# Kernel tuning notes

Measured on AMD Instinct MI355X. Metric: run time of the kernel, lower is better.

## Reference

```python
import jax, jax.numpy as jnp
import numpy as np

E = 400000          # total child edges in the ready batch
P = 100000          # number of parent nodes (segments)
D = 256             # 2 * model_dim


def setup_inputs() -> dict:
    key = jax.random.key(0)
    ks = jax.random.split(key, 6)
    child_hs = jax.random.normal(ks[0], (E, D), dtype=jnp.float32)
    child_cs = jax.random.normal(ks[1], (E, D), dtype=jnp.float32)
    segment_ids = jnp.sort(jax.random.randint(ks[2], (E,), 0, P))
    W_gates = jax.random.normal(ks[3], (D, 3 * D), dtype=jnp.float32) * (1.0 / np.sqrt(D))
    b_gates = jnp.zeros((3 * D,), dtype=jnp.float32)
    W_f = jax.random.normal(ks[4], (D, D), dtype=jnp.float32) * (1.0 / np.sqrt(D))
    b_f = jnp.zeros((D,), dtype=jnp.float32)
    return {
        "child_hs": child_hs,
        "child_cs": child_cs,
        "segment_ids": segment_ids,
        "num_segments": P,
        "W_gates": W_gates,
        "b_gates": b_gates,
        "W_f": W_f,
        "b_f": b_f,
    }


def reference(child_hs, child_cs, segment_ids, num_segments, W_gates, b_gates, W_f, b_f):
    # child_hs_sum per parent (segment reduce over children)
    hs_sum = jax.ops.segment_sum(child_hs, segment_ids, num_segments=num_segments)  # [P, D]
    # gates = Linear(2*model_dim -> 6*model_dim), chunk into i, o, g
    gates = hs_sum @ W_gates + b_gates                         # [P, 3D]
    i, o, g = jnp.split(gates, 3, axis=1)
    i, o, g = jax.nn.sigmoid(i), jax.nn.sigmoid(o), jnp.tanh(g)
    # per-child forget gates, fc = f * c, segment-reduced per parent
    f = jax.nn.sigmoid(child_hs @ W_f + b_f)                   # [E, D]
    fc = jax.ops.segment_sum(f * child_cs, segment_ids, num_segments=num_segments)  # [P, D]
    # child-sum LSTM update
    c = i * g + fc
    h = o * jnp.tanh(c)
    return h, c
```

## Files before the change

### kernel.cpp

```cpp
#include <hip/hip_runtime.h>
#include <hip/hip_bf16.h>

typedef __attribute__((ext_vector_type(8))) short short8;
typedef __attribute__((ext_vector_type(4))) float floatx4;

#define DD 256

__device__ __forceinline__ unsigned short f2bf(float f) {
    unsigned int u = __builtin_bit_cast(unsigned int, f);
    u += 0x7FFFu + ((u >> 16) & 1u);
    return (unsigned short)(u >> 16);
}

__device__ __forceinline__ float sigm(float x) { return 1.0f / (1.0f + __expf(-x)); }
__device__ __forceinline__ float tanh_fast(float x) { return 2.0f / (1.0f + __expf(-2.0f * x)) - 1.0f; }

__global__ void pack_weights(const float* __restrict__ W_f, const float* __restrict__ W_g,
                             unsigned short* __restrict__ WfT, unsigned short* __restrict__ WgT) {
    int idx = blockIdx.x * 256 + threadIdx.x;
    if (idx < 65536) {
        int n = idx >> 8, k = idx & 255;
        WfT[idx] = f2bf(W_f[k * 256 + n]);
    } else {
        int i2 = idx - 65536;
        int n = i2 >> 8, k = i2 & 255;
        WgT[i2] = f2bf(W_g[k * 768 + n]);
    }
}

__global__ void build_start(const int* __restrict__ seg, int E, int P, int* __restrict__ start) {
    int e = blockIdx.x * blockDim.x + threadIdx.x;
    if (e >= E) return;
    int s = seg[e];
    if (e == 0) {
        for (int p = 0; p <= s; ++p) start[p] = 0;
    } else {
        int sp = seg[e - 1];
        for (int p = sp + 1; p <= s; ++p) start[p] = e;
    }
    if (e == E - 1) {
        for (int p = s + 1; p <= P; ++p) start[p] = E;
    }
}

__global__ void hs_reduce(const float* __restrict__ child_hs, const int* __restrict__ start,
                          int P, float* __restrict__ hs_sum) {
    int wave = threadIdx.x >> 6, lane = threadIdx.x & 63;
    int p = blockIdx.x * 4 + wave;
    if (p >= P) return;
    int lo = start[p], hi = start[p + 1];
    float4 acc = make_float4(0.f, 0.f, 0.f, 0.f);
    const float4* src = (const float4*)child_hs;
    for (int e = lo; e < hi; ++e) {
        float4 v = src[(size_t)e * 64 + lane];
        acc.x += v.x; acc.y += v.y; acc.z += v.z; acc.w += v.w;
    }
    ((float4*)hs_sum)[(size_t)p * 64 + lane] = acc;
}

__global__ __launch_bounds__(256, 2) void gemm1_fc(
    const float* __restrict__ child_hs, const float* __restrict__ child_cs,
    const int* __restrict__ seg, const unsigned short* __restrict__ WfT,
    const float* __restrict__ b_f, float* __restrict__ fc, int E) {
    __shared__ __align__(16) unsigned short ldsB[8192];
    const int tid = threadIdx.x;
    const int w = tid >> 6, lane = tid & 63;
    const int nl = lane & 15, q = lane >> 4;
    const int e_base = blockIdx.x * 64 + w * 16;

    floatx4 acc[16];
#pragma unroll
    for (int t = 0; t < 16; ++t) acc[t] = (floatx4){0.f, 0.f, 0.f, 0.f};

    const float* Arow = child_hs + (size_t)(e_base + nl) * DD;

    for (int ks = 0; ks < 8; ++ks) {
#pragma unroll
        for (int r = 0; r < 4; ++r) {
            int chunk = tid + r * 256;
            int n = chunk >> 2, qb = chunk & 3;
            uint4 v = *(const uint4*)(WfT + n * 256 + ks * 32 + qb * 8);
            int dst = ((n >> 4) << 6) + (qb << 4) + (n & 15);
            ((uint4*)ldsB)[dst] = v;
        }
        float4 a0 = *(const float4*)(Arow + ks * 32 + q * 8);
        float4 a1 = *(const float4*)(Arow + ks * 32 + q * 8 + 4);
        short8 af;
        af[0] = (short)f2bf(a0.x); af[1] = (short)f2bf(a0.y);
        af[2] = (short)f2bf(a0.z); af[3] = (short)f2bf(a0.w);
        af[4] = (short)f2bf(a1.x); af[5] = (short)f2bf(a1.y);
        af[6] = (short)f2bf(a1.z); af[7] = (short)f2bf(a1.w);
        __syncthreads();
#pragma unroll
        for (int t = 0; t < 16; ++t) {
            short8 bf = ((const short8*)ldsB)[t * 64 + lane];
            acc[t] = __builtin_amdgcn_mfma_f32_16x16x32_bf16(af, bf, acc[t], 0, 0, 0);
        }
        __syncthreads();
    }

    int e0 = e_base + q * 4;
    int s0 = seg[e0], s1 = seg[e0 + 1], s2 = seg[e0 + 2], s3 = seg[e0 + 3];
#pragma unroll
    for (int t = 0; t < 16; ++t) {
        int n = t * 16 + nl;
        float bias = b_f[n];
        float v0 = sigm(acc[t][0] + bias) * child_cs[(size_t)(e0 + 0) * DD + n];
        float v1 = sigm(acc[t][1] + bias) * child_cs[(size_t)(e0 + 1) * DD + n];
        float v2 = sigm(acc[t][2] + bias) * child_cs[(size_t)(e0 + 2) * DD + n];
        float v3 = sigm(acc[t][3] + bias) * child_cs[(size_t)(e0 + 3) * DD + n];
        float a = v0; int s = s0;
        if (s1 == s) { a += v1; } else { atomicAdd(&fc[(size_t)s * DD + n], a); a = v1; s = s1; }
        if (s2 == s) { a += v2; } else { atomicAdd(&fc[(size_t)s * DD + n], a); a = v2; s = s2; }
        if (s3 == s) { a += v3; } else { atomicAdd(&fc[(size_t)s * DD + n], a); a = v3; s = s3; }
        atomicAdd(&fc[(size_t)s * DD + n], a);
    }
}

__global__ __launch_bounds__(512, 2) void gemm2_lstm(
    const float* __restrict__ hs_sum, const unsigned short* __restrict__ WgT,
    const float* __restrict__ b_g, float* __restrict__ h_out, float* __restrict__ c_out, int P) {
    __shared__ __align__(16) unsigned short ldsB[24576];
    const int tid = threadIdx.x;
    const int w = tid >> 6, lane = tid & 63;
    const int wr = w >> 2, wc = w & 3;
    const int nl = lane & 15, q = lane >> 4;
    const int p_base = blockIdx.x * 64;

    floatx4 acc[2][12];
#pragma unroll
    for (int rt = 0; rt < 2; ++rt)
#pragma unroll
        for (int t = 0; t < 12; ++t) acc[rt][t] = (floatx4){0.f, 0.f, 0.f, 0.f};

    const float* Arow0 = hs_sum + (size_t)(p_base + wr * 32 + nl) * DD;
    const float* Arow1 = Arow0 + (size_t)16 * DD;

    for (int ks = 0; ks < 8; ++ks) {
#pragma unroll
        for (int r = 0; r < 6; ++r) {
            int chunk = tid + r * 512;
            int n = chunk >> 2, qb = chunk & 3;
            uint4 v = *(const uint4*)(WgT + n * 256 + ks * 32 + qb * 8);
            int dst = ((n >> 4) << 6) + (qb << 4) + (n & 15);
            ((uint4*)ldsB)[dst] = v;
        }
        float4 a0 = *(const float4*)(Arow0 + ks * 32 + q * 8);
        float4 a1 = *(const float4*)(Arow0 + ks * 32 + q * 8 + 4);
        float4 a2 = *(const float4*)(Arow1 + ks * 32 + q * 8);
        float4 a3 = *(const float4*)(Arow1 + ks * 32 + q * 8 + 4);
        short8 af0, af1;
        af0[0] = (short)f2bf(a0.x); af0[1] = (short)f2bf(a0.y);
        af0[2] = (short)f2bf(a0.z); af0[3] = (short)f2bf(a0.w);
        af0[4] = (short)f2bf(a1.x); af0[5] = (short)f2bf(a1.y);
        af0[6] = (short)f2bf(a1.z); af0[7] = (short)f2bf(a1.w);
        af1[0] = (short)f2bf(a2.x); af1[1] = (short)f2bf(a2.y);
        af1[2] = (short)f2bf(a2.z); af1[3] = (short)f2bf(a2.w);
        af1[4] = (short)f2bf(a3.x); af1[5] = (short)f2bf(a3.y);
        af1[6] = (short)f2bf(a3.z); af1[7] = (short)f2bf(a3.w);
        __syncthreads();
#pragma unroll
        for (int cgl = 0; cgl < 4; ++cgl) {
#pragma unroll
            for (int part = 0; part < 3; ++part) {
                int t = part * 16 + (wc * 4 + cgl);
                short8 bf = ((const short8*)ldsB)[t * 64 + lane];
                acc[0][cgl * 3 + part] =
                    __builtin_amdgcn_mfma_f32_16x16x32_bf16(af0, bf, acc[0][cgl * 3 + part], 0, 0, 0);
                acc[1][cgl * 3 + part] =
                    __builtin_amdgcn_mfma_f32_16x16x32_bf16(af1, bf, acc[1][cgl * 3 + part], 0, 0, 0);
            }
        }
        __syncthreads();
    }

#pragma unroll
    for (int rt = 0; rt < 2; ++rt) {
#pragma unroll
        for (int cgl = 0; cgl < 4; ++cgl) {
            int n = (wc * 4 + cgl) * 16 + nl;
            float bi = b_g[n], bo = b_g[256 + n], bg = b_g[512 + n];
#pragma unroll
            for (int reg = 0; reg < 4; ++reg) {
                int p = p_base + wr * 32 + rt * 16 + q * 4 + reg;
                if (p < P) {
                    float I = acc[rt][cgl * 3 + 0][reg] + bi;
                    float O = acc[rt][cgl * 3 + 1][reg] + bo;
                    float G = acc[rt][cgl * 3 + 2][reg] + bg;
                    float iv = sigm(I), ov = sigm(O), gv = tanh_fast(G);
                    float c = iv * gv + c_out[(size_t)p * DD + n];
                    float hv = ov * tanh_fast(c);
                    h_out[(size_t)p * DD + n] = hv;
                    c_out[(size_t)p * DD + n] = c;
                }
            }
        }
    }
}

extern "C" void kernel_launch(void* const* d_in, const int* in_sizes, int n_in,
                              void* d_out, int out_size, void* d_ws, size_t ws_size,
                              hipStream_t stream) {
    const float* child_hs = (const float*)d_in[0];
    const float* child_cs = (const float*)d_in[1];
    const int*   seg      = (const int*)d_in[2];
    const float* W_gates  = (const float*)d_in[4];
    const float* b_gates  = (const float*)d_in[5];
    const float* W_f      = (const float*)d_in[6];
    const float* b_f      = (const float*)d_in[7];

    const int D = 256;
    const int E = in_sizes[0] / D;
    const int P = out_size / (2 * D);

    float* h_out = (float*)d_out;
    float* c_out = (float*)d_out + (size_t)P * D;

    unsigned short* WfT = (unsigned short*)d_ws;
    unsigned short* WgT = WfT + 65536;
    int* start = (int*)(WgT + 196608);

    hipMemsetAsync(c_out, 0, (size_t)P * D * sizeof(float), stream);

    pack_weights<<<1024, 256, 0, stream>>>(W_f, W_gates, WfT, WgT);
    build_start<<<(E + 255) / 256, 256, 0, stream>>>(seg, E, P, start);
    hs_reduce<<<(P + 3) / 4, 256, 0, stream>>>(child_hs, start, P, h_out);
    gemm1_fc<<<E / 64, 256, 0, stream>>>(child_hs, child_cs, seg, WfT, b_f, c_out, E);
    gemm2_lstm<<<(P + 63) / 64, 512, 0, stream>>>(h_out, WgT, b_gates, h_out, c_out, P);
}
```

Measured before the change: 1.402 ms.

## Stage weight tiles via direct global-to-LDS loads with double-buffered prefetch

Both GEMM kernels now copy the bf16 weight tiles into LDS with global_load_lds instead of moving them through registers. gemm1_fc adds a second LDS buffer so the next k-slice of weights and activations is prefetched while the MFMAs for the current slice run. gemm2_lstm issues the next slice's weight loads right after the compute barrier. The goal is to hide weight and activation load latency behind MFMA work. The cost is more LDS per block in gemm1 and reliance on the direct-to-LDS lane layout producing the same swizzle as before.

```diff
diff --git a/kernel.cpp b/kernel.cpp
--- a/kernel.cpp
+++ b/kernel.cpp
@@ -14,6 +14,21 @@
 
 __device__ __forceinline__ float sigm(float x) { return 1.0f / (1.0f + __expf(-x)); }
 __device__ __forceinline__ float tanh_fast(float x) { return 2.0f / (1.0f + __expf(-2.0f * x)) - 1.0f; }
+
+__device__ __forceinline__ short8 pack8(float4 a, float4 b) {
+    short8 r;
+    r[0] = (short)f2bf(a.x); r[1] = (short)f2bf(a.y);
+    r[2] = (short)f2bf(a.z); r[3] = (short)f2bf(a.w);
+    r[4] = (short)f2bf(b.x); r[5] = (short)f2bf(b.y);
+    r[6] = (short)f2bf(b.z); r[7] = (short)f2bf(b.w);
+    return r;
+}
+
+__device__ __forceinline__ void stage16(const unsigned short* g, unsigned short* l) {
+    __builtin_amdgcn_global_load_lds(
+        (const __attribute__((address_space(1))) unsigned int*)g,
+        (__attribute__((address_space(3))) unsigned int*)l, 16, 0, 0);
+}
 
 __global__ void pack_weights(const float* __restrict__ W_f, const float* __restrict__ W_g,
                              unsigned short* __restrict__ WfT, unsigned short* __restrict__ WgT) {
@@ -62,7 +77,7 @@
     const float* __restrict__ child_hs, const float* __restrict__ child_cs,
     const int* __restrict__ seg, const unsigned short* __restrict__ WfT,
     const float* __restrict__ b_f, float* __restrict__ fc, int E) {
-    __shared__ __align__(16) unsigned short ldsB[8192];
+    __shared__ __align__(16) unsigned short ldsB[2][8192];
     const int tid = threadIdx.x;
     const int w = tid >> 6, lane = tid & 63;
     const int nl = lane & 15, q = lane >> 4;
@@ -72,30 +87,35 @@
 #pragma unroll
     for (int t = 0; t < 16; ++t) acc[t] = (floatx4){0.f, 0.f, 0.f, 0.f};
 
-    const float* Arow = child_hs + (size_t)(e_base + nl) * DD;
+    const float* Arow = child_hs + (size_t)(e_base + nl) * DD + q * 8;
+    const unsigned short* Wsrc = WfT + ((w * 64 + nl) << 8) + q * 8;
+
+#pragma unroll
+    for (int r = 0; r < 4; ++r)
+        stage16(Wsrc + (r << 12), &ldsB[0][(w * 4 + r) << 9]);
+    float4 a0 = *(const float4*)(Arow);
+    float4 a1 = *(const float4*)(Arow + 4);
+    short8 af = pack8(a0, a1);
+    __syncthreads();
 
     for (int ks = 0; ks < 8; ++ks) {
-#pragma unroll
-        for (int r = 0; r < 4; ++r) {
-            int chunk = tid + r * 256;
-            int n = chunk >> 2, qb = chunk & 3;
-            uint4 v = *(const uint4*)(WfT + n * 256 + ks * 32 + qb * 8);
-            int dst = ((n >> 4) << 6) + (qb << 4) + (n & 15);
-            ((uint4*)ldsB)[dst] = v;
-        }
-        float4 a0 = *(const float4*)(Arow + ks * 32 + q * 8);
-        float4 a1 = *(const float4*)(Arow + ks * 32 + q * 8 + 4);
-        short8 af;
-        af[0] = (short)f2bf(a0.x); af[1] = (short)f2bf(a0.y);
-        af[2] = (short)f2bf(a0.z); af[3] = (short)f2bf(a0.w);
-        af[4] = (short)f2bf(a1.x); af[5] = (short)f2bf(a1.y);
-        af[6] = (short)f2bf(a1.z); af[7] = (short)f2bf(a1.w);
-        __syncthreads();
+        const unsigned short* lcur = ldsB[ks & 1];
+        float4 b0, b1;
+        if (ks < 7) {
+            unsigned short* lnxt = ldsB[(ks + 1) & 1];
+            const unsigned short* ws = Wsrc + (ks + 1) * 32;
+#pragma unroll
+            for (int r = 0; r < 4; ++r)
+                stage16(ws + (r << 12), &lnxt[(w * 4 + r) << 9]);
+            b0 = *(const float4*)(Arow + (ks + 1) * 32);
+            b1 = *(const float4*)(Arow + (ks + 1) * 32 + 4);
+        }
 #pragma unroll
         for (int t = 0; t < 16; ++t) {
-            short8 bf = ((const short8*)ldsB)[t * 64 + lane];
+            short8 bf = ((const short8*)lcur)[t * 64 + lane];
             acc[t] = __builtin_amdgcn_mfma_f32_16x16x32_bf16(af, bf, acc[t], 0, 0, 0);
         }
+        if (ks < 7) af = pack8(b0, b1);
         __syncthreads();
     }
 
@@ -133,31 +153,21 @@
 #pragma unroll
         for (int t = 0; t < 12; ++t) acc[rt][t] = (floatx4){0.f, 0.f, 0.f, 0.f};
 
-    const float* Arow0 = hs_sum + (size_t)(p_base + wr * 32 + nl) * DD;
+    const float* Arow0 = hs_sum + (size_t)(p_base + wr * 32 + nl) * DD + q * 8;
     const float* Arow1 = Arow0 + (size_t)16 * DD;
+    const unsigned short* Wsrc = WgT + ((w * 96 + nl) << 8) + q * 8;
+
+#pragma unroll
+    for (int r = 0; r < 6; ++r)
+        stage16(Wsrc + (r << 12), &ldsB[(w * 6 + r) << 9]);
 
     for (int ks = 0; ks < 8; ++ks) {
-#pragma unroll
-        for (int r = 0; r < 6; ++r) {
-            int chunk = tid + r * 512;
-            int n = chunk >> 2, qb = chunk & 3;
-            uint4 v = *(const uint4*)(WgT + n * 256 + ks * 32 + qb * 8);
-            int dst = ((n >> 4) << 6) + (qb << 4) + (n & 15);
-            ((uint4*)ldsB)[dst] = v;
-        }
-        float4 a0 = *(const float4*)(Arow0 + ks * 32 + q * 8);
-        float4 a1 = *(const float4*)(Arow0 + ks * 32 + q * 8 + 4);
-        float4 a2 = *(const float4*)(Arow1 + ks * 32 + q * 8);
-        float4 a3 = *(const float4*)(Arow1 + ks * 32 + q * 8 + 4);
-        short8 af0, af1;
-        af0[0] = (short)f2bf(a0.x); af0[1] = (short)f2bf(a0.y);
-        af0[2] = (short)f2bf(a0.z); af0[3] = (short)f2bf(a0.w);
-        af0[4] = (short)f2bf(a1.x); af0[5] = (short)f2bf(a1.y);
-        af0[6] = (short)f2bf(a1.z); af0[7] = (short)f2bf(a1.w);
-        af1[0] = (short)f2bf(a2.x); af1[1] = (short)f2bf(a2.y);
-        af1[2] = (short)f2bf(a2.z); af1[3] = (short)f2bf(a2.w);
-        af1[4] = (short)f2bf(a3.x); af1[5] = (short)f2bf(a3.y);
-        af1[6] = (short)f2bf(a3.z); af1[7] = (short)f2bf(a3.w);
+        float4 a0 = *(const float4*)(Arow0 + ks * 32);
+        float4 a1 = *(const float4*)(Arow0 + ks * 32 + 4);
+        float4 a2 = *(const float4*)(Arow1 + ks * 32);
+        float4 a3 = *(const float4*)(Arow1 + ks * 32 + 4);
+        short8 af0 = pack8(a0, a1);
+        short8 af1 = pack8(a2, a3);
         __syncthreads();
 #pragma unroll
         for (int cgl = 0; cgl < 4; ++cgl) {
@@ -172,6 +182,12 @@
             }
         }
         __syncthreads();
+        if (ks < 7) {
+            const unsigned short* ws = Wsrc + (ks + 1) * 32;
+#pragma unroll
+            for (int r = 0; r < 6; ++r)
+                stage16(ws + (r << 12), &ldsB[(w * 6 + r) << 9]);
+        }
     }
 
 #pragma unroll
```

New measurement: 1.401 ms. Within noise of the previous version (-0.1%).
